# Kernel optimization log

Hardware: AMD Instinct MI355X
Metric: run time of the kernel (lower is better)

The kernel has to match this reference:

```python
import jax, jax.numpy as jnp
import numpy as np

WORD_VOCAB = 100000
TAG_VOCAB = 50
WD = 300
TD = 100
EMB = WD + TD          # 400: LSTM input size AND hidden size
H = EMB
L = 512


def setup_inputs() -> dict:
    key = jax.random.key(0)
    ks = jax.random.split(key, 16)
    def p(k, shape):
        return jax.random.normal(k, shape, dtype=jnp.float32) * 0.05
    return {
        "words_idx_tensor": jax.random.randint(ks[0], (1, L), 0, WORD_VOCAB),
        "tags_idx_tensor": jax.random.randint(ks[1], (1, L), 0, TAG_VOCAB),
        "max_length": L,
        "word_emb": p(ks[2], (WORD_VOCAB, WD)),
        "tag_emb": p(ks[3], (TAG_VOCAB, TD)),
        # stacked [fwd, bwd] directions per layer (PyTorch LSTM gate order i,f,g,o)
        "w_ih_l0": p(ks[4], (2, 4 * H, EMB)),
        "w_hh_l0": p(ks[5], (2, 4 * H, H)),
        "b_ih_l0": p(ks[6], (2, 4 * H)),
        "b_hh_l0": p(ks[7], (2, 4 * H)),
        "w_ih_l1": p(ks[8], (2, 4 * H, 2 * H)),
        "w_hh_l1": p(ks[9], (2, 4 * H, H)),
        "b_ih_l1": p(ks[10], (2, 4 * H)),
        "b_hh_l1": p(ks[11], (2, 4 * H)),
        "fc1_w": p(ks[12], (1, 4 * H)),
        "fc1_b": p(ks[13], (1,)),
    }


def _lstm_dir(x, w_ih, w_hh, b_ih, b_hh, reverse):
    # x: [T, in]. Precompute input projections once (hoisted out of scan).
    xi = x @ w_ih.T + b_ih + b_hh  # [T, 4H]
    Hn = w_hh.shape[1]

    def step(carry, g_in):
        h, c = carry
        g = g_in + h @ w_hh.T
        i, f, gg, o = jnp.split(g, 4, axis=-1)
        c = jax.nn.sigmoid(f) * c + jax.nn.sigmoid(i) * jnp.tanh(gg)
        h = jax.nn.sigmoid(o) * jnp.tanh(c)
        return (h, c), h

    init = (jnp.zeros((Hn,), x.dtype), jnp.zeros((Hn,), x.dtype))
    _, hs = jax.lax.scan(step, init, xi, reverse=reverse)
    return hs  # [T, H]


def _bilstm(x, w_ih, w_hh, b_ih, b_hh):
    fwd = _lstm_dir(x, w_ih[0], w_hh[0], b_ih[0], b_hh[0], False)
    bwd = _lstm_dir(x, w_ih[1], w_hh[1], b_ih[1], b_hh[1], True)
    return jnp.concatenate([fwd, bwd], axis=-1)  # [T, 2H]


def reference(words_idx_tensor, tags_idx_tensor, max_length, word_emb, tag_emb,
              w_ih_l0, w_hh_l0, b_ih_l0, b_hh_l0,
              w_ih_l1, w_hh_l1, b_ih_l1, b_hh_l1,
              fc1_w, fc1_b):
    # Embedding lookup + concat; batch dim of size 1 squeezed (torch's
    # view(shape[1], shape[0], -1) yields [L, 1, emb] for the LSTM).
    x = jnp.concatenate([word_emb[words_idx_tensor[0]],
                         tag_emb[tags_idx_tensor[0]]], axis=-1)  # [L, EMB]

    h = _bilstm(x, w_ih_l0, w_hh_l0, b_ih_l0, b_hh_l0)   # [L, 2H]
    h = _bilstm(h, w_ih_l1, w_hh_l1, b_ih_l1, b_hh_l1)   # [L, 2H]

    # Pairwise edge scores: tanh(W @ [h_i; h_j] + b).
    # Split W into head/dep halves -> two small GEMMs + broadcast outer-sum,
    # avoiding the O(L^2 * 4H) concatenated feature tensor.
    two_h = fc1_w.shape[1] // 2
    s = h @ fc1_w[:, :two_h].T   # [L, 1]
    t = h @ fc1_w[:, two_h:].T   # [L, 1]
    scores = jnp.tanh(s[:, None, :] + t[None, :, :] + fc1_b)  # [L, L, 1]
    # torch stacks (i outer, j inner) -> [L*L, 1, 1]
    return scores.reshape(max_length * max_length, 1, 1)
```

## Files before the change

kernel.cpp:

```cpp
#include <hip/hip_runtime.h>

#define SEQ 512
#define HID 400
#define GATES 1600
#define E1 800
#define TEAM 10
#define RECGRID 160
#define XCH 8

__device__ __forceinline__ float bf2f(unsigned short u) {
    return __uint_as_float(((unsigned)u) << 16);
}
__device__ __forceinline__ unsigned short f2bf(float f) {
    unsigned u = __float_as_uint(f);
    u += 0x7FFFu + ((u >> 16) & 1u);
    return (unsigned short)(u >> 16);
}
__device__ __forceinline__ float sigm(float x) { return 1.f / (1.f + __expf(-x)); }
__device__ __forceinline__ float tanh_f(float x) {
    float xc = fminf(fmaxf(x, -15.f), 15.f);
    float e = __expf(2.f * xc);
    return (e - 1.f) / (e + 1.f);
}
__device__ __forceinline__ float loadx(const void* p, size_t i, int isbf) {
    return isbf ? bf2f(((const unsigned short*)p)[i]) : ((const float*)p)[i];
}

__global__ void detect_kernel(const unsigned short* __restrict__ wemb,
                              unsigned* __restrict__ dtf) {
    __shared__ int cnt;
    if (threadIdx.x == 0) cnt = 0;
    __syncthreads();
    int pass = 0;
    for (int i = 0; i < 8; ++i) {
        unsigned short u = wemb[threadIdx.x * 8 + i];
        int e = (u >> 7) & 0xFF;
        pass += (e >= 100 && e <= 130) ? 1 : 0;
    }
    atomicAdd(&cnt, pass);
    __syncthreads();
    if (threadIdx.x == 0) *dtf = (cnt >= 1843) ? 1u : 0u;
}

__global__ void embed_kernel(const int* __restrict__ words, const int* __restrict__ tags,
                             const void* __restrict__ wemb, const void* __restrict__ temb,
                             float* __restrict__ x ,
                             const unsigned* __restrict__ dtf) {
    int t = blockIdx.x;
    int w = words[t], g = tags[t];
    int isbf = (int)*dtf;
    for (int k = threadIdx.x; k < HID; k += blockDim.x) {
        float v = (k < 300) ? loadx(wemb, (size_t)w * 300 + k, isbf)
                            : loadx(temb, (size_t)g * 100 + (k - 300), isbf);
        x[(size_t)t * HID + k] = v;
    }
}

__global__ __launch_bounds__(256) void proj_kernel(
        const void* __restrict__ Araw, int tagged,
        const void* __restrict__ Wraw ,
        const void* __restrict__ bihRaw, const void* __restrict__ bhhRaw,
        float* __restrict__ xi ,
        int K, const unsigned* __restrict__ dtf) {
    const int isbf = (int)*dtf;
    __shared__ float As[16][132];
    __shared__ float Ws[16][68];
    int tid = threadIdx.x;
    int t0 = blockIdx.x * 128, n0 = blockIdx.y * 64, dir = blockIdx.z;
    int arow = tid >> 1, akoff = (tid & 1) * 8;
    int wrow = tid >> 2, wkoff = (tid & 3) * 4;
    int tx = (tid & 15) * 4;
    int ty = (tid >> 4) * 8;

    const float* Af = (const float*)Araw + (size_t)(t0 + arow) * K + akoff;
    const unsigned long long* At = (const unsigned long long*)Araw +
                                   (size_t)(t0 + arow) * K + akoff;
    size_t wbase = (size_t)(dir * GATES + n0 + wrow) * K + wkoff;
    const float* Wf = (const float*)Wraw + wbase;
    const unsigned short* Wh = (const unsigned short*)Wraw + wbase;

    float acc[8][4] = {};
    for (int k0 = 0; k0 < K; k0 += 16) {
        float av8[8];
        if (tagged) {
            ulonglong2 q0 = *(const ulonglong2*)(At + k0);
            ulonglong2 q1 = *(const ulonglong2*)(At + k0 + 2);
            ulonglong2 q2 = *(const ulonglong2*)(At + k0 + 4);
            ulonglong2 q3 = *(const ulonglong2*)(At + k0 + 6);
            av8[0] = __uint_as_float((unsigned)q0.x); av8[1] = __uint_as_float((unsigned)q0.y);
            av8[2] = __uint_as_float((unsigned)q1.x); av8[3] = __uint_as_float((unsigned)q1.y);
            av8[4] = __uint_as_float((unsigned)q2.x); av8[5] = __uint_as_float((unsigned)q2.y);
            av8[6] = __uint_as_float((unsigned)q3.x); av8[7] = __uint_as_float((unsigned)q3.y);
        } else {
            float4 a0 = *(const float4*)(Af + k0);
            float4 a1 = *(const float4*)(Af + k0 + 4);
            av8[0] = a0.x; av8[1] = a0.y; av8[2] = a0.z; av8[3] = a0.w;
            av8[4] = a1.x; av8[5] = a1.y; av8[6] = a1.z; av8[7] = a1.w;
        }
        float4 wv;
        if (isbf) {
            ushort4 w4 = *(const ushort4*)(Wh + k0);
            wv = make_float4(bf2f(w4.x), bf2f(w4.y), bf2f(w4.z), bf2f(w4.w));
        } else {
            wv = *(const float4*)(Wf + k0);
        }
        __syncthreads();
#pragma unroll
        for (int i = 0; i < 8; ++i) As[akoff + i][arow] = av8[i];
        Ws[wkoff + 0][wrow] = wv.x; Ws[wkoff + 1][wrow] = wv.y;
        Ws[wkoff + 2][wrow] = wv.z; Ws[wkoff + 3][wrow] = wv.w;
        __syncthreads();
#pragma unroll
        for (int kk = 0; kk < 16; ++kk) {
            float4 alo = *(const float4*)&As[kk][ty];
            float4 ahi = *(const float4*)&As[kk][ty + 4];
            float4 w4  = *(const float4*)&Ws[kk][tx];
            float av[8] = {alo.x, alo.y, alo.z, alo.w, ahi.x, ahi.y, ahi.z, ahi.w};
            float wvv[4] = {w4.x, w4.y, w4.z, w4.w};
#pragma unroll
            for (int i = 0; i < 8; ++i)
#pragma unroll
                for (int j = 0; j < 4; ++j)
                    acc[i][j] = fmaf(av[i], wvv[j], acc[i][j]);
        }
    }
    float bias[4];
#pragma unroll
    for (int j = 0; j < 4; ++j) {
        int n = n0 + tx + j;
        bias[j] = loadx(bihRaw, dir * GATES + n, isbf) + loadx(bhhRaw, dir * GATES + n, isbf);
    }
    float* xout = xi + (size_t)dir * SEQ * GATES;
#pragma unroll
    for (int i = 0; i < 8; ++i) {
        int t = t0 + ty + i;
        float4 o = make_float4(acc[i][0] + bias[0], acc[i][1] + bias[1],
                               acc[i][2] + bias[2], acc[i][3] + bias[3]);
        *(float4*)&xout[(size_t)t * GATES + n0 + tx] = o;
    }
}

struct SyncArea { unsigned cnt[8]; unsigned claim[2]; unsigned pad[6]; };

template <int ISBF>
__global__ __launch_bounds__(512, 2) void rec_kernel(
        const float* __restrict__ xi ,
        const void* __restrict__ whhRaw ,
        unsigned long long* __restrict__ hx ,
        unsigned tagbase, SyncArea* __restrict__ sy,
        const unsigned* __restrict__ dtf) {
    if (*(volatile const unsigned*)dtf != (unsigned)ISBF) return;

    int tid = threadIdx.x;
    __shared__ int role[2];
    if (tid == 0) {
        unsigned xcd = __builtin_amdgcn_s_getreg((3 << 11) | 20) & 0xFu;
        unsigned rank = atomicAdd(&sy->cnt[xcd], 1u);
        unsigned group = rank / TEAM;
        unsigned key = 1u + xcd * 64u + group;
        if ((rank % TEAM) == TEAM - 1) {
            unsigned prev = atomicCAS(&sy->claim[0], 0u, key);
            if (prev != 0u) atomicCAS(&sy->claim[1], 0u, key);
        }
        int dir = -1;
        while (dir < 0) {
            unsigned c0 = __hip_atomic_load(&sy->claim[0], __ATOMIC_RELAXED,
                                            __HIP_MEMORY_SCOPE_AGENT);
            unsigned c1 = __hip_atomic_load(&sy->claim[1], __ATOMIC_RELAXED,
                                            __HIP_MEMORY_SCOPE_AGENT);
            if (c0 == key) dir = 0;
            else if (c1 == key) dir = 1;
            else if (c0 != 0u && c1 != 0u) dir = 2;
        }
        role[0] = dir;
        role[1] = (int)(rank % TEAM);
    }
    __syncthreads();
    const int dir = role[0];
    const int wg  = role[1];
    if (dir == 2) return;

    const int chunk = tid & 15;
    const int rg    = tid >> 4;
    const int dirHID = dir * HID;

    __shared__ __align__(16) float hbuf[HID];
    __shared__ __align__(16) float partials[160][20];
    __shared__ __align__(16) float gates[160];
    __shared__ __align__(16) float xibuf[2][XCH][160];

    unsigned pk[5][13];
    float    wf[5][25];
#pragma unroll
    for (int r = 0; r < 5; ++r) {
        int lr = rg * 5 + r;
        int jj = lr >> 2, gg = lr & 3;
        int grow = gg * HID + wg * 40 + jj;
        size_t base = ((size_t)dir * GATES + grow) * HID + chunk * 25;
        if (ISBF) {
            const unsigned short* p = (const unsigned short*)whhRaw + base;
#pragma unroll
            for (int c2 = 0; c2 < 12; ++c2)
                pk[r][c2] = ((unsigned)p[2 * c2 + 1] << 16) | (unsigned)p[2 * c2];
            pk[r][12] = ((unsigned)p[24]) << 16;
        } else {
            const float* p = (const float*)whhRaw + base;
#pragma unroll
            for (int c = 0; c < 25; ++c) wf[r][c] = p[c];
        }
    }

    const float* xibase = xi + (size_t)dir * SEQ * GATES;
#pragma unroll
    for (int u = 0; u < 3; ++u) {
        int idx = tid + u * 512;
        if (idx < XCH * 160) {
            int s = idx / 160, rem = idx - s * 160;
            int G = rem / 40, j = rem - G * 40;
            int ts = dir ? (SEQ - 1 - s) : s;
            xibuf[0][s][rem] = xibase[(size_t)ts * GATES + G * HID + wg * 40 + j];
        }
    }

    float cstate = 0.f;
    size_t myelem = (size_t)dirHID + wg * 40 + tid;

#pragma unroll 1
    for (int k = 0; k < SEQ; ++k) {
        int t = dir ? (SEQ - 1 - k) : k;

        if (k > 0) {
            if (tid < HID) {
                const unsigned want = tagbase + (unsigned)k;
                int tprev = dir ? (t + 1) : (t - 1);
                const volatile unsigned long long* p =
                    (const volatile unsigned long long*)&hx[(size_t)tprev * E1 + dirHID + tid];
                unsigned long long w;
                do { w = *p; } while ((unsigned)(w >> 32) != want);
                hbuf[tid] = __uint_as_float((unsigned)w);
            }
        } else {
            if (tid < HID) hbuf[tid] = 0.f;
        }
        __syncthreads();

        float pf[3] = {0.f, 0.f, 0.f};
        const bool fetch = ((k & 7) == 0) && (k + XCH < SEQ);
        if (fetch) {
#pragma unroll
            for (int u = 0; u < 3; ++u) {
                int idx = tid + u * 512;
                if (idx < XCH * 160) {
                    int s = idx / 160, rem = idx - s * 160;
                    int G = rem / 40, j = rem - G * 40;
                    int ks = k + XCH + s;
                    int ts = dir ? (SEQ - 1 - ks) : ks;
                    pf[u] = xibase[(size_t)ts * GATES + G * HID + wg * 40 + j];
                }
            }
        }

        float acc[5] = {0.f, 0.f, 0.f, 0.f, 0.f};
        if (ISBF) {
#pragma unroll
            for (int c2 = 0; c2 < 12; ++c2) {
                float h0 = hbuf[chunk * 25 + 2 * c2];
                float h1 = hbuf[chunk * 25 + 2 * c2 + 1];
#pragma unroll
                for (int r = 0; r < 5; ++r) {
                    unsigned u = pk[r][c2];
                    acc[r] = fmaf(__uint_as_float(u << 16), h0, acc[r]);
                    acc[r] = fmaf(__uint_as_float(u & 0xffff0000u), h1, acc[r]);
                }
            }
            float h24 = hbuf[chunk * 25 + 24];
#pragma unroll
            for (int r = 0; r < 5; ++r)
                acc[r] = fmaf(__uint_as_float(pk[r][12]), h24, acc[r]);
        } else {
#pragma unroll
            for (int c = 0; c < 25; ++c) {
                float hv = hbuf[chunk * 25 + c];
#pragma unroll
                for (int r = 0; r < 5; ++r)
                    acc[r] = fmaf(wf[r][c], hv, acc[r]);
            }
        }
#pragma unroll
        for (int r = 0; r < 5; ++r) partials[rg * 5 + r][chunk] = acc[r];

        if (fetch) {
            int nb = ((k >> 3) + 1) & 1;
#pragma unroll
            for (int u = 0; u < 3; ++u) {
                int idx = tid + u * 512;
                if (idx < XCH * 160) {
                    int s = idx / 160, rem = idx - s * 160;
                    xibuf[nb][s][rem] = pf[u];
                }
            }
        }
        __syncthreads();

        if (tid < 160) {
            const float4* pr = (const float4*)&partials[tid][0];
            float4 p0 = pr[0], p1 = pr[1], p2 = pr[2], p3 = pr[3];
            float s = p0.x + p0.y + p0.z + p0.w
                    + p1.x + p1.y + p1.z + p1.w
                    + p2.x + p2.y + p2.z + p2.w
                    + p3.x + p3.y + p3.z + p3.w;
            gates[tid] = s + xibuf[(k >> 3) & 1][k & 7][(tid & 3) * 40 + (tid >> 2)];
        }
        __syncthreads();

        if (tid < 40) {
            float4 g4 = *(const float4*)&gates[tid * 4];
            float ig = sigm(g4.x), fg = sigm(g4.y), cg = tanh_f(g4.z), og = sigm(g4.w);
            cstate = fg * cstate + ig * cg;
            float hv = og * tanh_f(cstate);
            unsigned long long w =
                ((unsigned long long)(tagbase + (unsigned)k + 1u) << 32) |
                (unsigned long long)__float_as_uint(hv);
            *(volatile unsigned long long*)&hx[(size_t)t * E1 + myelem] = w;
        }
    }
}

__global__ void st_kernel(const unsigned long long* __restrict__ h1x ,
                          const void* __restrict__ fw ,
                          float* __restrict__ sv, float* __restrict__ tv,
                          const unsigned* __restrict__ dtf) {
    int i = blockIdx.x;
    int lane = threadIdx.x;
    int isbf = (int)*dtf;
    float s = 0.f, t = 0.f;
    for (int j = lane; j < E1; j += 64) {
        float hv = __uint_as_float((unsigned)h1x[(size_t)i * E1 + j]);
        s += hv * loadx(fw, j, isbf);
        t += hv * loadx(fw, E1 + j, isbf);
    }
#pragma unroll
    for (int o = 32; o > 0; o >>= 1) {
        s += __shfl_xor(s, o, 64);
        t += __shfl_xor(t, o, 64);
    }
    if (lane == 0) { sv[i] = s; tv[i] = t; }
}

__global__ void scores_kernel(const float* __restrict__ sv, const float* __restrict__ tv,
                              const void* __restrict__ fb, void* __restrict__ out,
                              const unsigned* __restrict__ dtf) {
    int idx = blockIdx.x * blockDim.x + threadIdx.x;
    int i = idx >> 9, j = idx & 511;
    int isbf = (int)*dtf;
    float v = tanh_f(sv[i] + tv[j] + loadx(fb, 0, isbf));
    if (isbf) ((unsigned short*)out)[idx] = f2bf(v);
    else      ((float*)out)[idx] = v;
}

static constexpr size_t OFF_X    = 0;
static constexpr size_t OFF_XI   = 819200;
static constexpr size_t OFF_SV   = 7372800;
static constexpr size_t OFF_TV   = 7374848;
static constexpr size_t OFF_DTF  = 7376896;
static constexpr size_t OFF_SYNC = 7376960;
static constexpr size_t OFF_HX   = 7377216;

extern "C" void kernel_launch(void* const* d_in, const int* in_sizes, int n_in,
                              void* d_out, int out_size, void* d_ws, size_t ws_size,
                              hipStream_t stream) {
    const int* words = (const int*)d_in[0];
    const int* tags  = (const int*)d_in[1];
    const void* wemb = d_in[3];
    const void* temb = d_in[4];
    const void* wih0 = d_in[5];
    const void* whh0 = d_in[6];
    const void* bih0 = d_in[7];
    const void* bhh0 = d_in[8];
    const void* wih1 = d_in[9];
    const void* whh1 = d_in[10];
    const void* bih1 = d_in[11];
    const void* bhh1 = d_in[12];
    const void* fw   = d_in[13];
    const void* fb   = d_in[14];

    char* ws = (char*)d_ws;
    float* x               = (float*)(ws + OFF_X);
    float* xi              = (float*)(ws + OFF_XI);
    float* sv              = (float*)(ws + OFF_SV);
    float* tv              = (float*)(ws + OFF_TV);
    unsigned* dtf          = (unsigned*)(ws + OFF_DTF);
    SyncArea* sync0        = (SyncArea*)(ws + OFF_SYNC);
    SyncArea* sync1        = (SyncArea*)(ws + OFF_SYNC + 64);
    unsigned long long* hx = (unsigned long long*)(ws + OFF_HX);

    hipMemsetAsync(ws + OFF_SYNC, 0, 128, stream);
    detect_kernel<<<1, 256, 0, stream>>>((const unsigned short*)wemb, dtf);
    embed_kernel<<<SEQ, 128, 0, stream>>>(words, tags, wemb, temb, x, dtf);

    proj_kernel<<<dim3(4, 25, 2), 256, 0, stream>>>(x, 0, wih0, bih0, bhh0, xi, HID, dtf);
    rec_kernel<1><<<RECGRID, 512, 0, stream>>>(xi, whh0, hx, 0u, sync0, dtf);
    rec_kernel<0><<<RECGRID, 512, 0, stream>>>(xi, whh0, hx, 0u, sync0, dtf);

    proj_kernel<<<dim3(4, 25, 2), 256, 0, stream>>>(hx, 1, wih1, bih1, bhh1, xi, E1, dtf);
    rec_kernel<1><<<RECGRID, 512, 0, stream>>>(xi, whh1, hx, 512u, sync1, dtf);
    rec_kernel<0><<<RECGRID, 512, 0, stream>>>(xi, whh1, hx, 512u, sync1, dtf);

    st_kernel<<<SEQ, 64, 0, stream>>>(hx, fw, sv, tv, dtf);
    scores_kernel<<<(SEQ * SEQ) / 256, 256, 0, stream>>>(sv, tv, fb, d_out, dtf);
}
```

Before: 2.011 ms.

## Split recurrent matvec per gate row across 4 lanes with shuffle reduction

The recurrent kernel now uses 640 threads per block. Each group of 4 lanes owns one gate row and holds a quarter of its weights (100 values) in registers. The partial sums are combined with warp shuffles, and the four gates are gathered with shuffles inside the wave. This removes the LDS partials/gates buffers and two __syncthreads per timestep on the serial critical path. In exchange, register pressure per thread rises, occupancy drops to one block per CU, and correctness of the hbuf reuse now depends on the cross-block handshake ordering.

```diff
diff --git a/kernel.cpp b/kernel.cpp
--- a/kernel.cpp
+++ b/kernel.cpp
@@ -143,7 +143,7 @@
 struct SyncArea { unsigned cnt[8]; unsigned claim[2]; unsigned pad[6]; };
 
 template <int ISBF>
-__global__ __launch_bounds__(512, 2) void rec_kernel(
+__global__ __launch_bounds__(640, 1) void rec_kernel(
         const float* __restrict__ xi ,
         const void* __restrict__ whhRaw ,
         unsigned long long* __restrict__ hx ,
@@ -180,40 +180,34 @@
     const int wg  = role[1];
     if (dir == 2) return;
 
-    const int chunk = tid & 15;
-    const int rg    = tid >> 4;
+    const int lr = tid >> 2;
+    const int c  = tid & 3;
+    const int gg = lr & 3, jj = lr >> 2;
+    const int grow = gg * HID + wg * 40 + jj;
     const int dirHID = dir * HID;
 
     __shared__ __align__(16) float hbuf[HID];
-    __shared__ __align__(16) float partials[160][20];
-    __shared__ __align__(16) float gates[160];
     __shared__ __align__(16) float xibuf[2][XCH][160];
 
-    unsigned pk[5][13];
-    float    wf[5][25];
-#pragma unroll
-    for (int r = 0; r < 5; ++r) {
-        int lr = rg * 5 + r;
-        int jj = lr >> 2, gg = lr & 3;
-        int grow = gg * HID + wg * 40 + jj;
-        size_t base = ((size_t)dir * GATES + grow) * HID + chunk * 25;
+    unsigned pk[50];
+    float    wf[100];
+    {
+        size_t base = ((size_t)dir * GATES + grow) * HID + c * 100;
         if (ISBF) {
-            const unsigned short* p = (const unsigned short*)whhRaw + base;
-#pragma unroll
-            for (int c2 = 0; c2 < 12; ++c2)
-                pk[r][c2] = ((unsigned)p[2 * c2 + 1] << 16) | (unsigned)p[2 * c2];
-            pk[r][12] = ((unsigned)p[24]) << 16;
+            const unsigned* p = (const unsigned*)whhRaw + (base >> 1);
+#pragma unroll
+            for (int i = 0; i < 50; ++i) pk[i] = p[i];
         } else {
             const float* p = (const float*)whhRaw + base;
 #pragma unroll
-            for (int c = 0; c < 25; ++c) wf[r][c] = p[c];
+            for (int i = 0; i < 100; ++i) wf[i] = p[i];
         }
     }
 
     const float* xibase = xi + (size_t)dir * SEQ * GATES;
 #pragma unroll
-    for (int u = 0; u < 3; ++u) {
-        int idx = tid + u * 512;
+    for (int u = 0; u < 2; ++u) {
+        int idx = tid + u * 640;
         if (idx < XCH * 160) {
             int s = idx / 160, rem = idx - s * 160;
             int G = rem / 40, j = rem - G * 40;
@@ -223,7 +217,9 @@
     }
 
     float cstate = 0.f;
-    size_t myelem = (size_t)dirHID + wg * 40 + tid;
+    const size_t myelem = (size_t)dirHID + wg * 40 + jj;
+    const int local = tid & 63;
+    const int gbase = local & 48;
 
 #pragma unroll 1
     for (int k = 0; k < SEQ; ++k) {
@@ -244,12 +240,12 @@
         }
         __syncthreads();
 
-        float pf[3] = {0.f, 0.f, 0.f};
+        float pf[2] = {0.f, 0.f};
         const bool fetch = ((k & 7) == 0) && (k + XCH < SEQ);
         if (fetch) {
 #pragma unroll
-            for (int u = 0; u < 3; ++u) {
-                int idx = tid + u * 512;
+            for (int u = 0; u < 2; ++u) {
+                int idx = tid + u * 640;
                 if (idx < XCH * 160) {
                     int s = idx / 160, rem = idx - s * 160;
                     int G = rem / 40, j = rem - G * 40;
@@ -260,68 +256,52 @@
             }
         }
 
-        float acc[5] = {0.f, 0.f, 0.f, 0.f, 0.f};
+        float acc = 0.f;
         if (ISBF) {
 #pragma unroll
-            for (int c2 = 0; c2 < 12; ++c2) {
-                float h0 = hbuf[chunk * 25 + 2 * c2];
-                float h1 = hbuf[chunk * 25 + 2 * c2 + 1];
-#pragma unroll
-                for (int r = 0; r < 5; ++r) {
-                    unsigned u = pk[r][c2];
-                    acc[r] = fmaf(__uint_as_float(u << 16), h0, acc[r]);
-                    acc[r] = fmaf(__uint_as_float(u & 0xffff0000u), h1, acc[r]);
-                }
-            }
-            float h24 = hbuf[chunk * 25 + 24];
-#pragma unroll
-            for (int r = 0; r < 5; ++r)
-                acc[r] = fmaf(__uint_as_float(pk[r][12]), h24, acc[r]);
-        } else {
-#pragma unroll
-            for (int c = 0; c < 25; ++c) {
-                float hv = hbuf[chunk * 25 + c];
-#pragma unroll
-                for (int r = 0; r < 5; ++r)
-                    acc[r] = fmaf(wf[r][c], hv, acc[r]);
-            }
-        }
-#pragma unroll
-        for (int r = 0; r < 5; ++r) partials[rg * 5 + r][chunk] = acc[r];
-
-        if (fetch) {
-            int nb = ((k >> 3) + 1) & 1;
-#pragma unroll
-            for (int u = 0; u < 3; ++u) {
-                int idx = tid + u * 512;
-                if (idx < XCH * 160) {
-                    int s = idx / 160, rem = idx - s * 160;
-                    xibuf[nb][s][rem] = pf[u];
-                }
-            }
-        }
-        __syncthreads();
-
-        if (tid < 160) {
-            const float4* pr = (const float4*)&partials[tid][0];
-            float4 p0 = pr[0], p1 = pr[1], p2 = pr[2], p3 = pr[3];
-            float s = p0.x + p0.y + p0.z + p0.w
-                    + p1.x + p1.y + p1.z + p1.w
-                    + p2.x + p2.y + p2.z + p2.w
-                    + p3.x + p3.y + p3.z + p3.w;
-            gates[tid] = s + xibuf[(k >> 3) & 1][k & 7][(tid & 3) * 40 + (tid >> 2)];
-        }
-        __syncthreads();
-
-        if (tid < 40) {
-            float4 g4 = *(const float4*)&gates[tid * 4];
-            float ig = sigm(g4.x), fg = sigm(g4.y), cg = tanh_f(g4.z), og = sigm(g4.w);
+            for (int i = 0; i < 50; ++i) {
+                float2 hp = *(const float2*)&hbuf[c * 100 + 2 * i];
+                unsigned u = pk[i];
+                acc = fmaf(__uint_as_float(u << 16), hp.x, acc);
+                acc = fmaf(__uint_as_float(u & 0xffff0000u), hp.y, acc);
+            }
+        } else {
+#pragma unroll
+            for (int i = 0; i < 50; ++i) {
+                float2 hp = *(const float2*)&hbuf[c * 100 + 2 * i];
+                acc = fmaf(wf[2 * i], hp.x, acc);
+                acc = fmaf(wf[2 * i + 1], hp.y, acc);
+            }
+        }
+
+        acc += __shfl_xor(acc, 1, 64);
+        acc += __shfl_xor(acc, 2, 64);
+        float rs = acc + xibuf[(k >> 3) & 1][k & 7][gg * 40 + jj];
+        float gi = __shfl(rs, gbase + 0,  64);
+        float gf = __shfl(rs, gbase + 4,  64);
+        float gc = __shfl(rs, gbase + 8,  64);
+        float go = __shfl(rs, gbase + 12, 64);
+
+        if ((tid & 15) == 0) {
+            float ig = sigm(gi), fg = sigm(gf), cg = tanh_f(gc), og = sigm(go);
             cstate = fg * cstate + ig * cg;
             float hv = og * tanh_f(cstate);
             unsigned long long w =
                 ((unsigned long long)(tagbase + (unsigned)k + 1u) << 32) |
                 (unsigned long long)__float_as_uint(hv);
             *(volatile unsigned long long*)&hx[(size_t)t * E1 + myelem] = w;
+        }
+
+        if (fetch) {
+            int nb = ((k >> 3) + 1) & 1;
+#pragma unroll
+            for (int u = 0; u < 2; ++u) {
+                int idx = tid + u * 640;
+                if (idx < XCH * 160) {
+                    int s = idx / 160, rem = idx - s * 160;
+                    xibuf[nb][s][rem] = pf[u];
+                }
+            }
         }
     }
 }
@@ -399,12 +379,12 @@
     embed_kernel<<<SEQ, 128, 0, stream>>>(words, tags, wemb, temb, x, dtf);
 
     proj_kernel<<<dim3(4, 25, 2), 256, 0, stream>>>(x, 0, wih0, bih0, bhh0, xi, HID, dtf);
-    rec_kernel<1><<<RECGRID, 512, 0, stream>>>(xi, whh0, hx, 0u, sync0, dtf);
-    rec_kernel<0><<<RECGRID, 512, 0, stream>>>(xi, whh0, hx, 0u, sync0, dtf);
+    rec_kernel<1><<<RECGRID, 640, 0, stream>>>(xi, whh0, hx, 0u, sync0, dtf);
+    rec_kernel<0><<<RECGRID, 640, 0, stream>>>(xi, whh0, hx, 0u, sync0, dtf);
 
     proj_kernel<<<dim3(4, 25, 2), 256, 0, stream>>>(hx, 1, wih1, bih1, bhh1, xi, E1, dtf);
-    rec_kernel<1><<<RECGRID, 512, 0, stream>>>(xi, whh1, hx, 512u, sync1, dtf);
-    rec_kernel<0><<<RECGRID, 512, 0, stream>>>(xi, whh1, hx, 512u, sync1, dtf);
+    rec_kernel<1><<<RECGRID, 640, 0, stream>>>(xi, whh1, hx, 512u, sync1, dtf);
+    rec_kernel<0><<<RECGRID, 640, 0, stream>>>(xi, whh1, hx, 512u, sync1, dtf);
 
     st_kernel<<<SEQ, 64, 0, stream>>>(hx, fw, sv, tv, dtf);
     scores_kernel<<<(SEQ * SEQ) / 256, 256, 0, stream>>>(sv, tv, fb, d_out, dtf);
```

New measurement: 2.363 ms. 17.5% more time.
